# Optimization experiments

Measured on AMD Instinct MI355X. Metric: run time of the kernel, lower is better.

The kernel has to match this reference:

```python
import jax, jax.numpy as jnp
import numpy as np

B, T, D = 64, 4096, 256


def setup_inputs() -> dict:
    key = jax.random.key(0)
    k0, k1, k2, k3 = jax.random.split(key, 4)
    q = jax.random.normal(k0, (B, D), dtype=jnp.float32)
    k = jax.random.normal(k1, (B, T, D), dtype=jnp.float32)
    m = jax.random.uniform(k2, (B, T), dtype=jnp.float32)
    # learned params: torch.rand init for weights, zeros for bias
    W = jax.random.uniform(k3, (D, D), dtype=jnp.float32)
    bias = jnp.zeros((1,), dtype=jnp.float32)
    return {"q": q, "k": k, "m": m, "W": W, "bias": bias}


def reference(q, k, m, W, bias):
    # mids = W @ q   (original repeats W over batch; a single einsum suffices)
    mids = jnp.einsum('de,be->bd', W, q)            # [B, D]
    # scores_bt = tanh(k_bt . mids_b + bias)
    scores = jnp.tanh(jnp.einsum('btd,bd->bt', k, mids) + bias)  # [B, T]
    # masked, max-stabilized softmax over time
    scores = scores - jnp.max(scores, axis=1, keepdims=True)
    e = jnp.exp(scores) * m
    attn = e / jnp.sum(e, axis=1, keepdims=True)
    return attn
```

## Files before the change

### kernel.cpp

```cpp
#include <hip/hip_runtime.h>
#include <math.h>


#define BB 64
#define TT 4096
#define DD 256
#define TBLKS 32
#define ROWS_PER_BLOCK (TT / TBLKS)
#define ROWS_PER_WAVE  (ROWS_PER_BLOCK / 4)

__global__ __launch_bounds__(256) void mids_kernel(const float* __restrict__ q,
                                                   const float* __restrict__ W,
                                                   float* __restrict__ mids) {
    const int b    = blockIdx.x;
    const int lane = threadIdx.x & 63;
    const int wave = threadIdx.x >> 6;
    const float4 qf = ((const float4*)(q + (size_t)b * DD))[lane];
    for (int i = 0; i < 64; ++i) {
        const int d = wave * 64 + i;
        const float4 wf = ((const float4*)(W + (size_t)d * DD))[lane];
        float p = wf.x * qf.x + wf.y * qf.y + wf.z * qf.z + wf.w * qf.w;
        #pragma unroll
        for (int off = 32; off; off >>= 1) p += __shfl_xor(p, off, 64);
        if (lane == 0) mids[b * DD + d] = p;
    }
}

__global__ __launch_bounds__(256) void scores_kernel(const float* __restrict__ k,
                                                     const float* __restrict__ mids,
                                                     const float* __restrict__ bias,
                                                     float* __restrict__ scores,
                                                     float* __restrict__ partmax) {
    const int b    = blockIdx.x;
    const int tb   = blockIdx.y;
    const int lane = threadIdx.x & 63;
    const int wave = threadIdx.x >> 6;
    const float bv = bias[0];
    const float4 mf = ((const float4*)(mids + (size_t)b * DD))[lane];
    const float* kb = k + (size_t)b * TT * DD;

    __shared__ float wmax[4];
    float lmax = -2.0f;
    const int t0 = tb * ROWS_PER_BLOCK + wave * ROWS_PER_WAVE;
    for (int i = 0; i < ROWS_PER_WAVE; ++i) {
        const int t = t0 + i;
        const float4 kf = ((const float4*)(kb + (size_t)t * DD))[lane];
        float p = kf.x * mf.x + kf.y * mf.y + kf.z * mf.z + kf.w * mf.w;
        #pragma unroll
        for (int off = 32; off; off >>= 1) p += __shfl_xor(p, off, 64);
        const float s = tanhf(p + bv);
        if (lane == 0) scores[b * TT + t] = s;
        lmax = fmaxf(lmax, s);
    }
    if (lane == 0) wmax[wave] = lmax;
    __syncthreads();
    if (threadIdx.x == 0) {
        const float mm = fmaxf(fmaxf(wmax[0], wmax[1]), fmaxf(wmax[2], wmax[3]));
        partmax[b * TBLKS + tb] = mm;
    }
}

__global__ __launch_bounds__(256) void softmax_kernel(const float* __restrict__ scores,
                                                      const float* __restrict__ m,
                                                      const float* __restrict__ partmax,
                                                      float* __restrict__ out) {
    const int b    = blockIdx.x;
    const int tid  = threadIdx.x;
    const int lane = tid & 63;
    const int wave = tid >> 6;
    __shared__ float red[5];

    if (wave == 0) {
        float mv = (lane < TBLKS) ? partmax[b * TBLKS + lane] : -2.0f;
        #pragma unroll
        for (int off = 32; off; off >>= 1) mv = fmaxf(mv, __shfl_xor(mv, off, 64));
        if (lane == 0) red[4] = mv;
    }
    __syncthreads();
    const float maxv = red[4];

    float local = 0.0f;
    for (int t = tid; t < TT; t += 256) {
        const float e = expf(scores[b * TT + t] - maxv) * m[b * TT + t];
        out[b * TT + t] = e;
        local += e;
    }
    #pragma unroll
    for (int off = 32; off; off >>= 1) local += __shfl_xor(local, off, 64);
    if (lane == 0) red[wave] = local;
    __syncthreads();
    const float inv = 1.0f / (red[0] + red[1] + red[2] + red[3]);

    for (int t = tid; t < TT; t += 256) out[b * TT + t] *= inv;
}

extern "C" void kernel_launch(void* const* d_in, const int* in_sizes, int n_in,
                              void* d_out, int out_size, void* d_ws, size_t ws_size,
                              hipStream_t stream) {
    const float* q    = (const float*)d_in[0];
    const float* k    = (const float*)d_in[1];
    const float* m    = (const float*)d_in[2];
    const float* W    = (const float*)d_in[3];
    const float* bias = (const float*)d_in[4];
    float* out = (float*)d_out;

    float* ws      = (float*)d_ws;
    float* mids    = ws;
    float* scores  = mids + BB * DD;
    float* partmax = scores + BB * TT;

    mids_kernel<<<BB, 256, 0, stream>>>(q, W, mids);
    scores_kernel<<<dim3(BB, TBLKS), 256, 0, stream>>>(k, mids, bias, scores, partmax);
    softmax_kernel<<<BB, 256, 0, stream>>>(scores, m, partmax, out);
}
```

Baseline: 431.2 us.

## Use 16-lane row groups, fast tanh, and split softmax across more blocks

The mids and scores kernels now let each 16-lane group handle one row, with a 4-step shuffle reduction, so one wave processes four rows at a time instead of one. The mids grid is split four ways across D. tanh is replaced by an exp- and rcp-based approximation. The single-block-per-batch softmax becomes an exp kernel plus a normalization kernel, each with 8 blocks per batch, which adds a launch but gives more parallelism.

```diff
diff --git a/kernel.cpp b/kernel.cpp
--- a/kernel.cpp
+++ b/kernel.cpp
@@ -6,23 +6,49 @@
 #define TT 4096
 #define DD 256
 #define TBLKS 32
-#define ROWS_PER_BLOCK (TT / TBLKS)
-#define ROWS_PER_WAVE  (ROWS_PER_BLOCK / 4)
+#define RPB (TT / TBLKS)
+#define GB 8
+#define CHUNK (TT / GB)
+
+__device__ __forceinline__ float fast_tanh(float x) {
+    float e = __expf(2.0f * x);
+    return 1.0f - 2.0f * __builtin_amdgcn_rcpf(1.0f + e);
+}
 
 __global__ __launch_bounds__(256) void mids_kernel(const float* __restrict__ q,
                                                    const float* __restrict__ W,
                                                    float* __restrict__ mids) {
     const int b    = blockIdx.x;
+    const int seg  = blockIdx.y;
     const int lane = threadIdx.x & 63;
     const int wave = threadIdx.x >> 6;
-    const float4 qf = ((const float4*)(q + (size_t)b * DD))[lane];
-    for (int i = 0; i < 64; ++i) {
-        const int d = wave * 64 + i;
-        const float4 wf = ((const float4*)(W + (size_t)d * DD))[lane];
-        float p = wf.x * qf.x + wf.y * qf.y + wf.z * qf.z + wf.w * qf.w;
-        #pragma unroll
-        for (int off = 32; off; off >>= 1) p += __shfl_xor(p, off, 64);
-        if (lane == 0) mids[b * DD + d] = p;
+    const int grp  = lane >> 4;
+    const int l16  = lane & 15;
+
+    const float* qb = q + (size_t)b * DD + l16 * 4;
+    const float4 qf0 = *(const float4*)(qb + 0);
+    const float4 qf1 = *(const float4*)(qb + 64);
+    const float4 qf2 = *(const float4*)(qb + 128);
+    const float4 qf3 = *(const float4*)(qb + 192);
+
+    const int d0 = seg * 64 + wave * 16;
+    #pragma unroll
+    for (int g = 0; g < 4; ++g) {
+        const int d = d0 + g * 4 + grp;
+        const float* wr = W + (size_t)d * DD + l16 * 4;
+        const float4 w0 = *(const float4*)(wr + 0);
+        const float4 w1 = *(const float4*)(wr + 64);
+        const float4 w2 = *(const float4*)(wr + 128);
+        const float4 w3 = *(const float4*)(wr + 192);
+        float p = w0.x*qf0.x + w0.y*qf0.y + w0.z*qf0.z + w0.w*qf0.w;
+        p += w1.x*qf1.x + w1.y*qf1.y + w1.z*qf1.z + w1.w*qf1.w;
+        p += w2.x*qf2.x + w2.y*qf2.y + w2.z*qf2.z + w2.w*qf2.w;
+        p += w3.x*qf3.x + w3.y*qf3.y + w3.z*qf3.z + w3.w*qf3.w;
+        p += __shfl_xor(p, 1, 64);
+        p += __shfl_xor(p, 2, 64);
+        p += __shfl_xor(p, 4, 64);
+        p += __shfl_xor(p, 8, 64);
+        if (l16 == 0) mids[b * DD + d] = p;
     }
 }
 
@@ -35,63 +61,101 @@
     const int tb   = blockIdx.y;
     const int lane = threadIdx.x & 63;
     const int wave = threadIdx.x >> 6;
+    const int grp  = lane >> 4;
+    const int l16  = lane & 15;
     const float bv = bias[0];
-    const float4 mf = ((const float4*)(mids + (size_t)b * DD))[lane];
-    const float* kb = k + (size_t)b * TT * DD;
 
+    const float* mb = mids + (size_t)b * DD + l16 * 4;
+    const float4 mf0 = *(const float4*)(mb + 0);
+    const float4 mf1 = *(const float4*)(mb + 64);
+    const float4 mf2 = *(const float4*)(mb + 128);
+    const float4 mf3 = *(const float4*)(mb + 192);
+
+    const int t0 = tb * RPB + wave * 32;
+    const float* kbase = k + ((size_t)b * TT + t0) * DD + l16 * 4;
+
+    float lmax = -2.0f;
+    #pragma unroll 2
+    for (int g = 0; g < 8; ++g) {
+        const int trow = g * 4 + grp;
+        const float* kr = kbase + (size_t)trow * DD;
+        const float4 k0 = *(const float4*)(kr + 0);
+        const float4 k1 = *(const float4*)(kr + 64);
+        const float4 k2 = *(const float4*)(kr + 128);
+        const float4 k3 = *(const float4*)(kr + 192);
+        float p = k0.x*mf0.x + k0.y*mf0.y + k0.z*mf0.z + k0.w*mf0.w;
+        p += k1.x*mf1.x + k1.y*mf1.y + k1.z*mf1.z + k1.w*mf1.w;
+        p += k2.x*mf2.x + k2.y*mf2.y + k2.z*mf2.z + k2.w*mf2.w;
+        p += k3.x*mf3.x + k3.y*mf3.y + k3.z*mf3.z + k3.w*mf3.w;
+        p += __shfl_xor(p, 1, 64);
+        p += __shfl_xor(p, 2, 64);
+        p += __shfl_xor(p, 4, 64);
+        p += __shfl_xor(p, 8, 64);
+        const float s = fast_tanh(p + bv);
+        lmax = fmaxf(lmax, s);
+        if (l16 == 0) scores[b * TT + t0 + trow] = s;
+    }
+    lmax = fmaxf(lmax, __shfl_xor(lmax, 16, 64));
+    lmax = fmaxf(lmax, __shfl_xor(lmax, 32, 64));
     __shared__ float wmax[4];
-    float lmax = -2.0f;
-    const int t0 = tb * ROWS_PER_BLOCK + wave * ROWS_PER_WAVE;
-    for (int i = 0; i < ROWS_PER_WAVE; ++i) {
-        const int t = t0 + i;
-        const float4 kf = ((const float4*)(kb + (size_t)t * DD))[lane];
-        float p = kf.x * mf.x + kf.y * mf.y + kf.z * mf.z + kf.w * mf.w;
-        #pragma unroll
-        for (int off = 32; off; off >>= 1) p += __shfl_xor(p, off, 64);
-        const float s = tanhf(p + bv);
-        if (lane == 0) scores[b * TT + t] = s;
-        lmax = fmaxf(lmax, s);
-    }
     if (lane == 0) wmax[wave] = lmax;
     __syncthreads();
-    if (threadIdx.x == 0) {
-        const float mm = fmaxf(fmaxf(wmax[0], wmax[1]), fmaxf(wmax[2], wmax[3]));
-        partmax[b * TBLKS + tb] = mm;
-    }
+    if (threadIdx.x == 0)
+        partmax[b * TBLKS + tb] =
+            fmaxf(fmaxf(wmax[0], wmax[1]), fmaxf(wmax[2], wmax[3]));
 }
 
-__global__ __launch_bounds__(256) void softmax_kernel(const float* __restrict__ scores,
-                                                      const float* __restrict__ m,
-                                                      const float* __restrict__ partmax,
-                                                      float* __restrict__ out) {
+__global__ __launch_bounds__(256) void exp_kernel(const float* __restrict__ scores,
+                                                  const float* __restrict__ m,
+                                                  const float* __restrict__ partmax,
+                                                  float* __restrict__ out,
+                                                  float* __restrict__ blocksum) {
     const int b    = blockIdx.x;
+    const int g    = blockIdx.y;
     const int tid  = threadIdx.x;
     const int lane = tid & 63;
     const int wave = tid >> 6;
-    __shared__ float red[5];
+    __shared__ float smax;
+    __shared__ float wsum[4];
 
     if (wave == 0) {
         float mv = (lane < TBLKS) ? partmax[b * TBLKS + lane] : -2.0f;
         #pragma unroll
-        for (int off = 32; off; off >>= 1) mv = fmaxf(mv, __shfl_xor(mv, off, 64));
-        if (lane == 0) red[4] = mv;
+        for (int off = 16; off; off >>= 1) mv = fmaxf(mv, __shfl_xor(mv, off, 64));
+        if (lane == 0) smax = mv;
     }
     __syncthreads();
-    const float maxv = red[4];
+    const float maxv = smax;
 
-    float local = 0.0f;
-    for (int t = tid; t < TT; t += 256) {
-        const float e = expf(scores[b * TT + t] - maxv) * m[b * TT + t];
-        out[b * TT + t] = e;
-        local += e;
-    }
+    const int idx = b * TT + g * CHUNK + tid * 2;
+    const float2 sv = *(const float2*)(scores + idx);
+    const float2 mv2 = *(const float2*)(m + idx);
+    const float e0 = __expf(sv.x - maxv) * mv2.x;
+    const float e1 = __expf(sv.y - maxv) * mv2.y;
+    *(float2*)(out + idx) = make_float2(e0, e1);
+
+    float local = e0 + e1;
     #pragma unroll
     for (int off = 32; off; off >>= 1) local += __shfl_xor(local, off, 64);
-    if (lane == 0) red[wave] = local;
+    if (lane == 0) wsum[wave] = local;
     __syncthreads();
-    const float inv = 1.0f / (red[0] + red[1] + red[2] + red[3]);
+    if (tid == 0)
+        blocksum[b * GB + g] = wsum[0] + wsum[1] + wsum[2] + wsum[3];
+}
 
-    for (int t = tid; t < TT; t += 256) out[b * TT + t] *= inv;
+__global__ __launch_bounds__(256) void norm_kernel(const float* __restrict__ blocksum,
+                                                   float* __restrict__ out) {
+    const int b   = blockIdx.x;
+    const int g   = blockIdx.y;
+    const int tid = threadIdx.x;
+    float s = 0.0f;
+    #pragma unroll
+    for (int i = 0; i < GB; ++i) s += blocksum[b * GB + i];
+    const float inv = 1.0f / s;
+    const int idx = b * TT + g * CHUNK + tid * 2;
+    float2 v = *(const float2*)(out + idx);
+    v.x *= inv; v.y *= inv;
+    *(float2*)(out + idx) = v;
 }
 
 extern "C" void kernel_launch(void* const* d_in, const int* in_sizes, int n_in,
@@ -104,12 +168,14 @@
     const float* bias = (const float*)d_in[4];
     float* out = (float*)d_out;
 
-    float* ws      = (float*)d_ws;
-    float* mids    = ws;
-    float* scores  = mids + BB * DD;
-    float* partmax = scores + BB * TT;
+    float* ws       = (float*)d_ws;
+    float* mids     = ws;
+    float* scores   = mids + BB * DD;
+    float* partmax  = scores + BB * TT;
+    float* blocksum = partmax + BB * TBLKS;
 
-    mids_kernel<<<BB, 256, 0, stream>>>(q, W, mids);
+    mids_kernel<<<dim3(BB, 4), 256, 0, stream>>>(q, W, mids);
     scores_kernel<<<dim3(BB, TBLKS), 256, 0, stream>>>(k, mids, bias, scores, partmax);
-    softmax_kernel<<<BB, 256, 0, stream>>>(scores, m, partmax, out);
+    exp_kernel<<<dim3(BB, GB), 256, 0, stream>>>(scores, m, partmax, out, blocksum);
+    norm_kernel<<<dim3(BB, GB), 256, 0, stream>>>(blocksum, out);
 }
```

New measurement: 398.1 us. -7.7%, faster.
